# Kernel optimization log

Hardware: AMD Instinct MI355X
Metric: run time of the kernel (lower is better)

The kernel has to match this reference:

```python
import jax, jax.numpy as jnp
import numpy as np

B, L, N = 8, 5, 4096
RADIUS, K = 0.7, 32
SPATIAL_STRIDE = 16
TK, TSTRIDE = 3, 2  # temporal kernel / stride; temporal_padding=[1,1] replicate
DIM, DEPTH, HEADS, DIM_HEAD, MLP_DIM, OUT_DIM = 512, 5, 8, 64, 1024, 1088
INNER = HEADS * DIM_HEAD
N_ANCH = 64
NTOT = N + N_ANCH
M = NTOT // SPATIAL_STRIDE  # spatial anchors per output frame


def setup_inputs() -> dict:
    key = jax.random.key(0)
    ks = list(jax.random.split(key, 16))
    s = 0.02
    p = {}
    p["points"] = jax.random.uniform(ks[0], (B, L, N, 3), jnp.float32, -1.0, 1.0)
    p["conv_d_w"] = jax.random.normal(ks[1], (DIM, 4), jnp.float32) * s
    p["conv_f_w"] = jax.random.normal(ks[2], (DIM, 3), jnp.float32) * s
    p["pos_w"] = jax.random.normal(ks[3], (DIM, 4), jnp.float32) * s
    p["pos_b"] = jnp.zeros((DIM,), jnp.float32)
    p["ln1_g"] = jnp.ones((DEPTH, DIM)); p["ln1_b"] = jnp.zeros((DEPTH, DIM))
    p["qkv_w"] = jax.random.normal(ks[4], (DEPTH, DIM, 3 * INNER), jnp.float32) * s
    p["attn_out_w"] = jax.random.normal(ks[5], (DEPTH, INNER, DIM), jnp.float32) * s
    p["attn_out_b"] = jnp.zeros((DEPTH, DIM))
    p["ln2_g"] = jnp.ones((DEPTH, DIM)); p["ln2_b"] = jnp.zeros((DEPTH, DIM))
    p["ff1_w"] = jax.random.normal(ks[6], (DEPTH, DIM, MLP_DIM), jnp.float32) * s
    p["ff1_b"] = jnp.zeros((DEPTH, MLP_DIM))
    p["ff2_w"] = jax.random.normal(ks[7], (DEPTH, MLP_DIM, DIM), jnp.float32) * s
    p["ff2_b"] = jnp.zeros((DEPTH, DIM))
    p["head_ln_g"] = jnp.ones((DIM,)); p["head_ln_b"] = jnp.zeros((DIM,))
    p["head1_w"] = jax.random.normal(ks[8], (DIM, MLP_DIM), jnp.float32) * s
    p["head1_b"] = jnp.zeros((MLP_DIM,))
    p["head2_w"] = jax.random.normal(ks[9], (MLP_DIM, OUT_DIM), jnp.float32) * s
    p["head2_b"] = jnp.zeros((OUT_DIM,))
    return p


def _layer_norm(x, g, b, eps=1e-5):
    mu = jnp.mean(x, -1, keepdims=True)
    var = jnp.mean((x - mu) ** 2, -1, keepdims=True)
    return (x - mu) * jax.lax.rsqrt(var + eps) * g + b


def _anchor_grid():
    lin = jnp.linspace(-1.5, 1.5, 4)
    gx, gy, gz = jnp.meshgrid(lin, lin, lin, indexing="ij")
    return jnp.stack([gx.ravel(), gy.ravel(), gz.ravel()], -1)  # (64,3)


def _fps(pts, m):
    # furthest point sampling, pts (N,3) -> (m,) int32, first pick is index 0 (pointnet2 semantics)
    def step(carry, _):
        dist, last = carry
        d = jnp.sum((pts - pts[last]) ** 2, -1)
        dist = jnp.minimum(dist, d)
        return (dist, jnp.argmax(dist).astype(jnp.int32)), last
    init = (jnp.full((pts.shape[0],), 1e10, pts.dtype), jnp.int32(0))
    _, idx = jax.lax.scan(step, init, None, length=m)
    return idx


def _ball_query(anchors, pts, radius, k):
    # first k point indices within radius of each anchor; pad with first hit (0 if none)
    d2 = jnp.sum((anchors[:, None, :] - pts[None, :, :]) ** 2, -1)  # (M,N)
    n = pts.shape[0]
    cand = jnp.where(d2 < radius * radius, jnp.arange(n, dtype=jnp.int32), n)
    neg_topk, _ = jax.lax.top_k(-cand, k)  # k smallest indices, ascending
    idx = -neg_topk
    first = idx[:, :1]
    idx = jnp.where(idx == n, first, idx)
    return jnp.where(idx == n, 0, idx)


def _forward(points, conv_d_w, conv_f_w, pos_w, pos_b, ln1_g, ln1_b, qkv_w,
             attn_out_w, attn_out_b, ln2_g, ln2_b, ff1_w, ff1_b, ff2_w, ff2_b,
             head_ln_g, head_ln_b, head1_w, head1_b, head2_w, head2_b):
    anch = _anchor_grid()  # (64,3)
    pts = jnp.concatenate(
        [points[..., :3], jnp.broadcast_to(anch, (B, L, N_ANCH, 3))], axis=2)  # (B,L,NTOT,3)
    # replicate temporal padding [1,1]
    frames = jnp.concatenate([pts[:, :1], pts, pts[:, -1:]], axis=1)  # (B,L+2,NTOT,3)

    trad = (TK - 1) // 2
    nT = L + 2
    gather = jax.vmap(lambda p, i: p[i])
    out_xyz, out_feat = [], []
    for t in range(trad, nT - trad, TSTRIDE):
        f_t = frames[:, t]                                   # (B,NTOT,3)
        a_idx = jax.vmap(lambda p: _fps(p, M))(f_t)          # (B,M)
        a_xyz = gather(f_t, a_idx)                           # (B,M,3)
        feats_w = []
        for i in range(t - trad, t + trad + 1):
            nb = frames[:, i]                                # (B,NTOT,3)
            idx = jax.vmap(lambda a, p: _ball_query(a, p, RADIUS, K))(a_xyz, nb)  # (B,M,K)
            grouped = gather(nb, idx)                        # (B,M,K,3)
            disp = grouped - a_xyz[:, :, None, :]
            tdisp = jnp.full((B, M, K, 1), float(i - t), disp.dtype)
            disp4 = jnp.concatenate([disp, tdisp], -1)       # (B,M,K,4)
            # conv_f(features) + conv_d(displacement); features fed in are the xyz themselves
            feat = (jnp.einsum("bmkc,dc->bmkd", grouped, conv_f_w)
                    + jnp.einsum("bmkc,dc->bmkd", disp4, conv_d_w))
            feats_w.append(jnp.max(feat, axis=2))            # spatial max -> (B,M,DIM)
        out_feat.append(jnp.max(jnp.stack(feats_w, 0), axis=0))  # temporal max
        out_xyz.append(a_xyz)

    nF = len(out_xyz)
    xyzs = jnp.stack(out_xyz, 1)                             # (B,nF,M,3)
    feats = jnp.stack(out_feat, 1).reshape(B, nF * M, DIM)
    tcol = jnp.broadcast_to(
        jnp.arange(1, nF + 1, dtype=xyzs.dtype)[None, :, None, None], (B, nF, M, 1))
    xyzts = jnp.concatenate([xyzs, tcol], -1).reshape(B, nF * M, 4)
    x = jnp.einsum("bnc,dc->bnd", xyzts, pos_w) + pos_b + feats  # (B,T,DIM); emb_relu=False

    scale = DIM_HEAD ** -0.5
    for l in range(DEPTH):
        xn = _layer_norm(x, ln1_g[l], ln1_b[l])
        q, k, v = jnp.split(xn @ qkv_w[l], 3, axis=-1)
        rs = lambda a: a.reshape(B, -1, HEADS, DIM_HEAD)
        q, k, v = rs(q), rs(k), rs(v)
        att = jax.nn.softmax(jnp.einsum("bqhd,bkhd->bhqk", q, k) * scale, axis=-1)
        o = jnp.einsum("bhqk,bkhd->bqhd", att, v).reshape(B, -1, INNER)
        x = x + o @ attn_out_w[l] + attn_out_b[l]
        xn = _layer_norm(x, ln2_g[l], ln2_b[l])
        x = x + jax.nn.gelu(xn @ ff1_w[l] + ff1_b[l], approximate=False) @ ff2_w[l] + ff2_b[l]

    x = jnp.max(x, axis=1)                                   # (B,DIM)
    x = _layer_norm(x, head_ln_g, head_ln_b)
    x = jax.nn.gelu(x @ head1_w + head1_b, approximate=False) @ head2_w + head2_b
    x = x.reshape(B, 1, OUT_DIM // 64, 64)
    x = jax.nn.softmax(x, axis=-1)
    return x @ anch                                          # (B,1,J,3)


def reference(points, conv_d_w, conv_f_w, pos_w, pos_b, ln1_g, ln1_b, qkv_w,
              attn_out_w, attn_out_b, ln2_g, ln2_b, ff1_w, ff1_b, ff2_w, ff2_b,
              head_ln_g, head_ln_b, head1_w, head1_b, head2_w, head2_b):
    return _forward(points, conv_d_w, conv_f_w, pos_w, pos_b, ln1_g, ln1_b, qkv_w,
                    attn_out_w, attn_out_b, ln2_g, ln2_b, ff1_w, ff1_b, ff2_w, ff2_b,
                    head_ln_g, head_ln_b, head1_w, head1_b, head2_w, head2_b)
```

## Files before the change

### kernel.cpp

```cpp
#include <hip/hip_runtime.h>
#include <hip/hip_bf16.h>
#include <cstddef>

#define BB 8
#define LL 5
#define NN 4096
#define NANCH 64
#define NPTS 4160
#define MM 260
#define NFRAME 3
#define SSEQ 780
#define DIMC 512
#define NHEAD 8
#define DHEAD 64
#define MLPD 1024
#define OUTD 1088
#define NROWS 6240
#define VPITCH 784
#define WBUFSZ 2097152

typedef __attribute__((ext_vector_type(8))) short s16x8;
typedef __attribute__((ext_vector_type(4))) float fx4;
typedef unsigned short ushort_t;
typedef unsigned int uint_t;

__device__ __forceinline__ float sqdist_rn(float x1, float y1, float z1,
                                           float x2, float y2, float z2) {
    float dx = __fsub_rn(x1, x2);
    float dy = __fsub_rn(y1, y2);
    float dz = __fsub_rn(z1, z2);
    return __fadd_rn(__fadd_rn(__fmul_rn(dx, dx), __fmul_rn(dy, dy)), __fmul_rn(dz, dz));
}

__device__ __forceinline__ float gelu_exact(float v) {
    return 0.5f * v * (1.0f + erff(v * 0.70710678118654752440f));
}

__device__ __forceinline__ uint_t bf16rn(float f) {
    uint_t u = __float_as_uint(f);
    return (u + 0x7FFFu + ((u >> 16) & 1u)) >> 16;
}
__device__ __forceinline__ void split2(float f, ushort_t& h, ushort_t& l) {
    uint_t hb = bf16rn(f);
    h = (ushort_t)hb;
    float fh = __uint_as_float(hb << 16);
    l = (ushort_t)bf16rn(f - fh);
}

typedef __attribute__((address_space(3))) unsigned int as3u;
typedef const __attribute__((address_space(1))) unsigned int as1u;
__device__ __forceinline__ void gload16(const ushort_t* g, ushort_t* l) {
    __builtin_amdgcn_global_load_lds((as1u*)g, (as3u*)l, 16, 0, 0);
}

template <int CTRL>
__device__ __forceinline__ int dpp_mov(int v) {
    return __builtin_amdgcn_update_dpp(0, v, CTRL, 0xF, 0xF, true);
}
#define DPP_STEP_F(op, v, ctrl) v = op(v, __int_as_float(dpp_mov<ctrl>(__float_as_int(v))))
__device__ __forceinline__ float wave_max_bcast(float v) {
    DPP_STEP_F(fmaxf, v, 0x111); DPP_STEP_F(fmaxf, v, 0x112);
    DPP_STEP_F(fmaxf, v, 0x114); DPP_STEP_F(fmaxf, v, 0x118);
    DPP_STEP_F(fmaxf, v, 0x142); DPP_STEP_F(fmaxf, v, 0x143);
    return __int_as_float(__builtin_amdgcn_readlane(__float_as_int(v), 63));
}
__device__ __forceinline__ float faddf(float a, float b) { return a + b; }
__device__ __forceinline__ float wave_sum_bcast(float v) {
    DPP_STEP_F(faddf, v, 0x111); DPP_STEP_F(faddf, v, 0x112);
    DPP_STEP_F(faddf, v, 0x114); DPP_STEP_F(faddf, v, 0x118);
    DPP_STEP_F(faddf, v, 0x142); DPP_STEP_F(faddf, v, 0x143);
    return __int_as_float(__builtin_amdgcn_readlane(__float_as_int(v), 63));
}
__device__ __forceinline__ float row16_maxf(float v) {
    DPP_STEP_F(fmaxf, v, 0x111); DPP_STEP_F(fmaxf, v, 0x112);
    DPP_STEP_F(fmaxf, v, 0x114); DPP_STEP_F(fmaxf, v, 0x118);
    return __int_as_float(__builtin_amdgcn_readlane(__float_as_int(v), 15));
}

__device__ __forceinline__ void wsplit_tile(
    int bid, int tid, int nthr,
    const float* __restrict__ qkvw, const float* __restrict__ projw,
    const float* __restrict__ ff1w, const float* __restrict__ ff2w,
    ushort_t* __restrict__ th, ushort_t* __restrict__ tl,
    float (*T)[33]) {
    const float* src; int K, N; size_t dst;
    if (bid < 768)       { src = qkvw;  K = 512;  N = 1536; dst = 0;       }
    else if (bid < 1024) { src = projw; K = 512;  N = 512;  dst = 786432;  bid -= 768;  }
    else if (bid < 1536) { src = ff1w;  K = 512;  N = 1024; dst = 1048576; bid -= 1024; }
    else                 { src = ff2w;  K = 1024; N = 512;  dst = 1572864; bid -= 1536; }
    int ntn = N >> 5;
    int tn = bid % ntn, tk = bid / ntn;
    int n0 = tn * 32, k0 = tk * 32;
    for (int e = tid; e < 1024; e += nthr) {
        int r = e >> 5, c = e & 31;
        T[r][c] = src[(size_t)(k0 + r) * N + n0 + c];
    }
    __syncthreads();
    for (int e = tid; e < 1024; e += nthr) {
        int r = e >> 5, c = e & 31;
        ushort_t h, l;
        split2(T[c][r], h, l);
        th[dst + (size_t)(n0 + r) * K + k0 + c] = h;
        tl[dst + (size_t)(n0 + r) * K + k0 + c] = l;
    }
}

__global__ __launch_bounds__(256) void build_pts_kernel(const float* __restrict__ points,
                                                        float* __restrict__ pts) {
    int i = blockIdx.x * 256 + threadIdx.x;
    if (i >= BB * LL * NPTS) return;
    int n = i % NPTS;
    int bl = i / NPTS;
    if (n < NN) {
        const float* src = points + ((size_t)bl * NN + n) * 3;
        pts[(size_t)i * 3 + 0] = src[0];
        pts[(size_t)i * 3 + 1] = src[1];
        pts[(size_t)i * 3 + 2] = src[2];
    } else {
        int j = n - NN;
        int ix = j >> 4, iy = (j >> 2) & 3, iz = j & 3;
        pts[(size_t)i * 3 + 0] = -1.5f + (float)ix;
        pts[(size_t)i * 3 + 1] = -1.5f + (float)iy;
        pts[(size_t)i * 3 + 2] = -1.5f + (float)iz;
    }
}

__global__ __launch_bounds__(256) void fps_ws_kernel(
    const float* __restrict__ pts, float* __restrict__ axyz,
    const float* __restrict__ qkvw, const float* __restrict__ projw,
    const float* __restrict__ ff1w, const float* __restrict__ ff2w,
    ushort_t* __restrict__ th, ushort_t* __restrict__ tl) {
    __shared__ __align__(16) char smem[50048];
    int bid = blockIdx.x;
    int tid = threadIdx.x;
    if (bid >= 24) {
        wsplit_tile(bid - 24, tid, 256, qkvw, projw, ff1w, ff2w, th, tl,
                    (float(*)[33])smem);
        return;
    }
    float* sx = (float*)smem;
    float* sy = sx + NPTS;
    float* sz = sy + NPTS;
    float* redv = sz + NPTS;
    int* redi = (int*)(redv + 8);

    int b = bid / 3, f = bid % 3;
    const float* P = pts + (size_t)(b * LL + 2 * f) * NPTS * 3;
    int lane = tid & 63, wid = tid >> 6;
    int start = tid < 64 ? 17 * tid : 1088 + 16 * (tid - 64);
    float px[17], py[17], pz[17], dist[17];
#pragma unroll
    for (int j = 0; j < 16; j++) {
        int n = start + j;
        float gx = P[(size_t)n * 3 + 0];
        float gy = P[(size_t)n * 3 + 1];
        float gz = P[(size_t)n * 3 + 2];
        px[j] = gx; py[j] = gy; pz[j] = gz;
        sx[n] = gx; sy[n] = gy; sz[n] = gz;
        dist[j] = 1e10f;
    }
    if (tid < 64) {
        int n = start + 16;
        float gx = P[(size_t)n * 3 + 0];
        float gy = P[(size_t)n * 3 + 1];
        float gz = P[(size_t)n * 3 + 2];
        px[16] = gx; py[16] = gy; pz[16] = gz;
        sx[n] = gx; sy[n] = gy; sz[n] = gz;
        dist[16] = 1e10f;
    } else {
        px[16] = 0.f; py[16] = 0.f; pz[16] = 0.f;
        dist[16] = -1.0f;
    }
    __syncthreads();
    float ax = sx[0], ay = sy[0], az = sz[0];
    float* out = axyz + (size_t)bid * MM * 3;
    for (int m = 0; m < MM; m++) {
        if (tid == 0) { out[m * 3 + 0] = ax; out[m * 3 + 1] = ay; out[m * 3 + 2] = az; }
        float bv = -1.0f;
        int bjn = start;
#pragma unroll
        for (int j = 0; j < 16; j++) {
            float d = sqdist_rn(px[j], py[j], pz[j], ax, ay, az);
            float dj = fminf(dist[j], d);
            dist[j] = dj;
            if (dj > bv) { bv = dj; bjn = start + j; }
        }
        if (tid < 64) {
            float d = sqdist_rn(px[16], py[16], pz[16], ax, ay, az);
            float dj = fminf(dist[16], d);
            dist[16] = dj;
            if (dj > bv) { bv = dj; bjn = start + 16; }
        }
        float wmv = wave_max_bcast(bv);
        unsigned long long mk = __ballot(bv == wmv);
        int srcl = __ffsll(mk) - 1;
        int wn = __builtin_amdgcn_readlane(bjn, srcl);
        int par = (m & 1) * 4;
        if (lane == 0) { redv[par + wid] = wmv; redi[par + wid] = wn; }
        __syncthreads();
        float b0 = redv[par + 0], b1 = redv[par + 1];
        float b2 = redv[par + 2], b3 = redv[par + 3];
        int i0 = redi[par + 0], i1 = redi[par + 1];
        int i2 = redi[par + 2], i3 = redi[par + 3];
        float bb = b0; int bn = i0;
        if (b1 > bb) { bb = b1; bn = i1; }
        if (b2 > bb) { bb = b2; bn = i2; }
        if (b3 > bb) { bb = b3; bn = i3; }
        ax = sx[bn]; ay = sy[bn]; az = sz[bn];
    }
}

__global__ __launch_bounds__(64) void group_conv_kernel(
    const float* __restrict__ pts, const float* __restrict__ axyz,
    const float* __restrict__ conv_d_w, const float* __restrict__ conv_f_w,
    const float* __restrict__ pos_w, const float* __restrict__ pos_b,
    float* __restrict__ x) {
    int gid = blockIdx.x;
    int b = gid / SSEQ;
    int rem = gid % SSEQ;
    int f = rem / MM;
    int lane = threadIdx.x;
    const float* A = axyz + (size_t)gid * 3;
    float ax = A[0], ay = A[1], az = A[2];

    float cf0[8], cf1[8], cf2[8], cd0[8], cd1[8], cd2[8], cd3[8], fmx[8];
#pragma unroll
    for (int c = 0; c < 8; c++) {
        int d = lane + 64 * c;
        cf0[c] = conv_f_w[d * 3 + 0];
        cf1[c] = conv_f_w[d * 3 + 1];
        cf2[c] = conv_f_w[d * 3 + 2];
        cd0[c] = conv_d_w[d * 4 + 0];
        cd1[c] = conv_d_w[d * 4 + 1];
        cd2[c] = conv_d_w[d * 4 + 2];
        cd3[c] = conv_d_w[d * 4 + 3];
        fmx[c] = -INFINITY;
    }
    __shared__ int nbr[32];
    __shared__ float gxs[32], gys[32], gzs[32];
    const float R2 = 0.49000000953674316f;

    for (int wi = 0; wi < 3; wi++) {
        int l = 2 * f + wi - 1;
        l = l < 0 ? 0 : (l > 4 ? 4 : l);
        const float* P = pts + (size_t)(b * LL + l) * NPTS * 3;
        int cnt = 0;
        for (int base = 0; base < NPTS && cnt < 32; base += 64) {
            int n = base + lane;
            float d2 = sqdist_rn(P[(size_t)n * 3], P[(size_t)n * 3 + 1], P[(size_t)n * 3 + 2],
                                 ax, ay, az);
            bool hit = d2 < R2;
            unsigned long long mk = __ballot(hit);
            int rank = (int)__popcll(mk & (((unsigned long long)1 << lane) - 1ull));
            if (hit && (cnt + rank) < 32) nbr[cnt + rank] = n;
            cnt += (int)__popcll(mk);
        }
        __syncthreads();
        int eff = cnt < 32 ? cnt : 32;
        if (lane < 32) {
            int idx = (eff == 0) ? 0 : (lane < eff ? nbr[lane] : nbr[0]);
            gxs[lane] = P[(size_t)idx * 3 + 0];
            gys[lane] = P[(size_t)idx * 3 + 1];
            gzs[lane] = P[(size_t)idx * 3 + 2];
        }
        __syncthreads();
        float tf = (float)(wi - 1);
        for (int k = 0; k < 32; k++) {
            float gx = gxs[k], gy = gys[k], gz = gzs[k];
            float dx = gx - ax, dy = gy - ay, dz = gz - az;
#pragma unroll
            for (int c = 0; c < 8; c++) {
                float v = gx * cf0[c] + gy * cf1[c] + gz * cf2[c] +
                          dx * cd0[c] + dy * cd1[c] + dz * cd2[c] + tf * cd3[c];
                fmx[c] = fmaxf(fmx[c], v);
            }
        }
        __syncthreads();
    }
    float tcol = (float)(f + 1);
#pragma unroll
    for (int c = 0; c < 8; c++) {
        int d = lane + 64 * c;
        float pos = ax * pos_w[d * 4 + 0] + ay * pos_w[d * 4 + 1] +
                    az * pos_w[d * 4 + 2] + tcol * pos_w[d * 4 + 3] + pos_b[d];
        x[(size_t)gid * DIMC + d] = fmx[c] + pos;
    }
}

__global__ __launch_bounds__(64) void ln_kernel(const float* __restrict__ x,
                                                const float* __restrict__ g,
                                                const float* __restrict__ b,
                                                ushort_t* __restrict__ yh,
                                                ushort_t* __restrict__ yl) {
    int r = blockIdx.x;
    int lane = threadIdx.x;
    const float* xr = x + (size_t)r * DIMC;
    float4 v0 = *(const float4*)(xr + lane * 8);
    float4 v1 = *(const float4*)(xr + lane * 8 + 4);
    float s = v0.x + v0.y + v0.z + v0.w + v1.x + v1.y + v1.z + v1.w;
    s = wave_sum_bcast(s);
    float mean = s * (1.0f / 512.0f);
    float dv[8];
    dv[0] = v0.x - mean; dv[1] = v0.y - mean; dv[2] = v0.z - mean; dv[3] = v0.w - mean;
    dv[4] = v1.x - mean; dv[5] = v1.y - mean; dv[6] = v1.z - mean; dv[7] = v1.w - mean;
    float sq = 0.f;
#pragma unroll
    for (int c = 0; c < 8; c++) sq += dv[c] * dv[c];
    sq = wave_sum_bcast(sq);
    float var = sq * (1.0f / 512.0f);
    float inv = 1.0f / sqrtf(var + 1e-5f);
    int d = lane * 8;
    ushort_t hs[8], ls[8];
#pragma unroll
    for (int c = 0; c < 8; c++) {
        float v = dv[c] * inv * g[d + c] + b[d + c];
        split2(v, hs[c], ls[c]);
    }
    uint4 hv, lv;
    hv.x = hs[0] | ((uint_t)hs[1] << 16); hv.y = hs[2] | ((uint_t)hs[3] << 16);
    hv.z = hs[4] | ((uint_t)hs[5] << 16); hv.w = hs[6] | ((uint_t)hs[7] << 16);
    lv.x = ls[0] | ((uint_t)ls[1] << 16); lv.y = ls[2] | ((uint_t)ls[3] << 16);
    lv.z = ls[4] | ((uint_t)ls[5] << 16); lv.w = ls[6] | ((uint_t)ls[7] << 16);
    *(uint4*)(yh + (size_t)r * DIMC + d) = hv;
    *(uint4*)(yl + (size_t)r * DIMC + d) = lv;
}

#define BK 32

template <int BN, int EPI>
__global__ __launch_bounds__(256) void gemm_mfma(
    const ushort_t* __restrict__ Ahg, const ushort_t* __restrict__ Alg,
    const ushort_t* __restrict__ Bhg, const ushort_t* __restrict__ Blg,
    const float* __restrict__ bias, const float* __restrict__ R,
    float* __restrict__ C, ushort_t* __restrict__ Ch, ushort_t* __restrict__ Cl,
    ushort_t* __restrict__ Vh, ushort_t* __restrict__ Vl,
    int M, int N, int K) {
    const int WN = BN / 2, NT = WN / 16;
    __shared__ __align__(16) ushort_t Ah[128 * BK];
    __shared__ __align__(16) ushort_t Al[128 * BK];
    __shared__ __align__(16) ushort_t Bh[BN * BK];
    __shared__ __align__(16) ushort_t Bl[BN * BK];
    int tid = threadIdx.x;
    int lane = tid & 63, w = tid >> 6;
    int wm = w & 1, wn = w >> 1;
    int quad = lane >> 4, l15 = lane & 15;

    int nx = gridDim.x;
    int nwg = nx * gridDim.y;
    int lid = blockIdx.x + nx * blockIdx.y;
    int q = nwg >> 3, r = nwg & 7;
    int xcd = lid & 7, off = lid >> 3;
    int nid = (xcd < r ? xcd * (q + 1) : r * (q + 1) + (xcd - r) * q) + off;
    int m0 = (nid / nx) * 128, n0 = (nid % nx) * BN;

    int sr = lane >> 2;
    int sc = lane & 3;
    int kq = ((sc ^ ((sr >> 1) & 3)) << 3);

    int aoff[2];
#pragma unroll
    for (int i = 0; i < 2; i++) {
        int g = w + 4 * i;
        int row = m0 + g * 16 + sr; if (row >= M) row = M - 1;
        aoff[i] = row * K + kq;
    }
    int boff[BN == 128 ? 2 : 1];
    if (BN == 128) {
#pragma unroll
        for (int i = 0; i < 2; i++) {
            int g = w + 4 * i;
            boff[i] = (n0 + g * 16 + sr) * K + kq;
        }
    } else {
        boff[0] = (n0 + w * 16 + sr) * K + kq;
    }

    fx4 acc[4][NT];
#pragma unroll
    for (int mi = 0; mi < 4; mi++)
#pragma unroll
        for (int nj = 0; nj < NT; nj++) acc[mi][nj] = (fx4){0.f, 0.f, 0.f, 0.f};

    int rsw = (l15 >> 1) & 3;
    int aro = (64 * wm + l15) * BK + ((quad ^ rsw) << 3);
    int bro = (WN * wn + l15) * BK + ((quad ^ rsw) << 3);

    for (int k0 = 0; k0 < K; k0 += BK) {
#pragma unroll
        for (int i = 0; i < 2; i++) {
            int g = w + 4 * i;
            gload16(Ahg + aoff[i] + k0, &Ah[g * 16 * BK]);
            gload16(Alg + aoff[i] + k0, &Al[g * 16 * BK]);
        }
        if (BN == 128) {
#pragma unroll
            for (int i = 0; i < 2; i++) {
                int g = w + 4 * i;
                gload16(Bhg + boff[i] + k0, &Bh[g * 16 * BK]);
                gload16(Blg + boff[i] + k0, &Bl[g * 16 * BK]);
            }
        } else {
            gload16(Bhg + boff[0] + k0, &Bh[w * 16 * BK]);
            gload16(Blg + boff[0] + k0, &Bl[w * 16 * BK]);
        }
        __syncthreads();

        s16x8 bf[NT][2];
#pragma unroll
        for (int nj = 0; nj < NT; nj++) {
            bf[nj][0] = *(const s16x8*)&Bh[bro + 16 * nj * BK];
            bf[nj][1] = *(const s16x8*)&Bl[bro + 16 * nj * BK];
        }
#pragma unroll
        for (int mi = 0; mi < 4; mi++) {
            s16x8 aH = *(const s16x8*)&Ah[aro + 16 * mi * BK];
            s16x8 aL = *(const s16x8*)&Al[aro + 16 * mi * BK];
#pragma unroll
            for (int nj = 0; nj < NT; nj++) {
                acc[mi][nj] = __builtin_amdgcn_mfma_f32_16x16x32_bf16(aH, bf[nj][0], acc[mi][nj], 0, 0, 0);
                acc[mi][nj] = __builtin_amdgcn_mfma_f32_16x16x32_bf16(aH, bf[nj][1], acc[mi][nj], 0, 0, 0);
                acc[mi][nj] = __builtin_amdgcn_mfma_f32_16x16x32_bf16(aL, bf[nj][0], acc[mi][nj], 0, 0, 0);
            }
        }
        __syncthreads();
    }
#pragma unroll
    for (int mi = 0; mi < 4; mi++) {
#pragma unroll
        for (int r2 = 0; r2 < 4; r2++) {
            int row = m0 + 64 * wm + 16 * mi + quad * 4 + r2;
            if (row < M) {
#pragma unroll
                for (int nj = 0; nj < NT; nj++) {
                    int col = n0 + WN * wn + 16 * nj + l15;
                    float v = acc[mi][nj][r2];
                    if (EPI == 0) {
                        C[(size_t)row * N + col] = v;
                    } else if (EPI == 3) {
                        C[(size_t)row * N + col] = v + bias[col] + R[(size_t)row * N + col];
                    } else if (EPI == 2) {
                        float gv = gelu_exact(v + bias[col]);
                        ushort_t h, l;
                        split2(gv, h, l);
                        Ch[(size_t)row * N + col] = h;
                        Cl[(size_t)row * N + col] = l;
                    } else if (EPI == 5) {
                        ushort_t h, l;
                        split2(v, h, l);
                        if (col < 1024) {
                            Ch[(size_t)row * 1024 + col] = h;
                            Cl[(size_t)row * 1024 + col] = l;
                        } else {
                            int bb = row / SSEQ, key = row % SSEQ;
                            int hh = (col - 1024) >> 6, dd = (col - 1024) & 63;
                            size_t vo = ((size_t)((bb * 8 + hh) * 64 + dd)) * VPITCH + key;
                            Vh[vo] = h;
                            Vl[vo] = l;
                        }
                    }
                }
            }
        }
    }
}

#define KP2 64
#define PP 72
#define NATTN 832

__global__ __launch_bounds__(256, 2) void attn_mfma_kernel(
    const ushort_t* __restrict__ qkh, const ushort_t* __restrict__ qkl,
    const ushort_t* __restrict__ vth, const ushort_t* __restrict__ vtl,
    ushort_t* __restrict__ oh, ushort_t* __restrict__ ol,
    const float* __restrict__ nqkvw, const float* __restrict__ nprojw,
    const float* __restrict__ nff1w, const float* __restrict__ nff2w,
    ushort_t* __restrict__ nth, ushort_t* __restrict__ ntl) {
    __shared__ __align__(16) char smem[67584];
    int lid = blockIdx.x;
    if (lid >= NATTN) {
        wsplit_tile(lid - NATTN, threadIdx.x, 256, nqkvw, nprojw, nff1w, nff2w,
                    nth, ntl, (float(*)[33])smem);
        return;
    }
    int xcd = lid & 7, idx = lid >> 3;
    int qt = idx % 13;
    int bh = xcd * 8 + idx / 13;
    int b = bh >> 3, h = bh & 7;

    ushort_t* Qh  = (ushort_t*)smem;
    ushort_t* Ql  = Qh + 64 * KP2;
    ushort_t* Kh  = Ql + 64 * KP2;
    ushort_t* Kl  = Kh + 64 * KP2;
    ushort_t* Vth = Kl + 64 * KP2;
    ushort_t* Vtl = Vth + 64 * KP2;
    ushort_t* Ph  = Vtl + 64 * KP2;
    ushort_t* Pl  = Ph + 64 * PP;

    int tid = threadIdx.x;
    int lane = tid & 63, w = tid >> 6;
    int quad = lane >> 4, l15 = lane & 15;

    int q0 = qt * 64;
    int nq = SSEQ - q0; if (nq > 64) nq = 64;

    int sr8 = lane >> 3;
    int csw = (lane & 7) ^ sr8;

#pragma unroll
    for (int i = 0; i < 2; i++) {
        int grp = i * 4 + w;
        int row = grp * 8 + sr8;
        int gq = q0 + (row < nq ? row : nq - 1);
        size_t go = (size_t)(b * SSEQ + gq) * 1024 + h * 64 + csw * 8;
        gload16(qkh + go, Qh + grp * 512);
        gload16(qkl + go, Ql + grp * 512);
    }

    fx4 accO[4];
#pragma unroll
    for (int dj = 0; dj < 4; dj++) accO[dj] = (fx4){0.f, 0.f, 0.f, 0.f};
    fx4 accL = (fx4){0.f, 0.f, 0.f, 0.f};

    s16x8 ones;
#pragma unroll
    for (int j = 0; j < 8; j++) ones[j] = (short)16256;

    int r7 = l15 & 7;
    int c0 = (quad ^ r7) * 8;
    int c1 = ((quad ^ r7) ^ 4) * 8;

    for (int kt = 0; kt < 13; kt++) {
        int k0 = kt * 64;
        int nk = SSEQ - k0; if (nk > 64) nk = 64;
        __syncthreads();
#pragma unroll
        for (int i = 0; i < 2; i++) {
            int grp = i * 4 + w;
            int row = grp * 8 + sr8;
            int gk = k0 + (row < nk ? row : nk - 1);
            size_t go = (size_t)(b * SSEQ + gk) * 1024 + h * 64 + 512 + csw * 8;
            gload16(qkh + go, Kh + grp * 512);
            gload16(qkl + go, Kl + grp * 512);
            size_t vo = ((size_t)(bh * 64 + row)) * VPITCH + k0 + csw * 8;
            gload16(vth + vo, Vth + grp * 512);
            gload16(vtl + vo, Vtl + grp * 512);
        }
        __syncthreads();

        fx4 accS[4];
#pragma unroll
        for (int nj = 0; nj < 4; nj++) accS[nj] = (fx4){0.f, 0.f, 0.f, 0.f};
#pragma unroll
        for (int ks = 0; ks < 2; ks++) {
            int ca = ks ? c1 : c0;
            s16x8 aH = *(const s16x8*)&Qh[(16 * w + l15) * KP2 + ca];
            s16x8 aL = *(const s16x8*)&Ql[(16 * w + l15) * KP2 + ca];
#pragma unroll
            for (int nj = 0; nj < 4; nj++) {
                s16x8 bH = *(const s16x8*)&Kh[(16 * nj + l15) * KP2 + ca];
                s16x8 bL = *(const s16x8*)&Kl[(16 * nj + l15) * KP2 + ca];
                accS[nj] = __builtin_amdgcn_mfma_f32_16x16x32_bf16(aH, bH, accS[nj], 0, 0, 0);
                accS[nj] = __builtin_amdgcn_mfma_f32_16x16x32_bf16(aH, bL, accS[nj], 0, 0, 0);
                accS[nj] = __builtin_amdgcn_mfma_f32_16x16x32_bf16(aL, bH, accS[nj], 0, 0, 0);
            }
        }
#pragma unroll
        for (int nj = 0; nj < 4; nj++) {
            int key = 16 * nj + l15;
            bool valid = key < nk;
#pragma unroll
            for (int r = 0; r < 4; r++) {
                float s = accS[nj][r] * 0.125f;
                float p = valid ? __expf(s) : 0.f;
                ushort_t hh, ll;
                split2(p, hh, ll);
                int qrow = 16 * w + quad * 4 + r;
                Ph[qrow * PP + key] = hh;
                Pl[qrow * PP + key] = ll;
            }
        }
#pragma unroll
        for (int ks = 0; ks < 2; ks++) {
            int ca = ks ? c1 : c0;
            s16x8 aPh = *(const s16x8*)&Ph[(16 * w + l15) * PP + 32 * ks + quad * 8];
            s16x8 aPl = *(const s16x8*)&Pl[(16 * w + l15) * PP + 32 * ks + quad * 8];
            accL = __builtin_amdgcn_mfma_f32_16x16x32_bf16(aPh, ones, accL, 0, 0, 0);
            accL = __builtin_amdgcn_mfma_f32_16x16x32_bf16(aPl, ones, accL, 0, 0, 0);
#pragma unroll
            for (int dj = 0; dj < 4; dj++) {
                s16x8 bVh = *(const s16x8*)&Vth[(16 * dj + l15) * KP2 + ca];
                s16x8 bVl = *(const s16x8*)&Vtl[(16 * dj + l15) * KP2 + ca];
                accO[dj] = __builtin_amdgcn_mfma_f32_16x16x32_bf16(aPh, bVh, accO[dj], 0, 0, 0);
                accO[dj] = __builtin_amdgcn_mfma_f32_16x16x32_bf16(aPh, bVl, accO[dj], 0, 0, 0);
                accO[dj] = __builtin_amdgcn_mfma_f32_16x16x32_bf16(aPl, bVh, accO[dj], 0, 0, 0);
            }
        }
    }
#pragma unroll
    for (int r = 0; r < 4; r++) {
        int lq = 16 * w + quad * 4 + r;
        if (lq < nq) {
            float inv = 1.0f / accL[r];
            size_t base = (size_t)(b * SSEQ + q0 + lq) * DIMC + h * 64 + l15;
#pragma unroll
            for (int dj = 0; dj < 4; dj++) {
                ushort_t hh, ll;
                split2(accO[dj][r] * inv, hh, ll);
                oh[base + 16 * dj] = hh;
                ol[base + 16 * dj] = ll;
            }
        }
    }
}

__global__ __launch_bounds__(512) void pool_max_kernel(const float* __restrict__ x,
                                                       float* __restrict__ partial) {
    int c = blockIdx.x;
    int bb = blockIdx.y;
    int d = threadIdx.x;
    const float* xb = x + ((size_t)(bb * SSEQ + c * 60)) * DIMC + d;
    float m = -INFINITY;
#pragma unroll 4
    for (int s = 0; s < 60; s++) m = fmaxf(m, xb[(size_t)s * DIMC]);
    partial[((size_t)bb * 13 + c) * DIMC + d] = m;
}

__global__ __launch_bounds__(512) void pool_ln_kernel(const float* __restrict__ partial,
                                                      const float* __restrict__ g,
                                                      const float* __restrict__ b,
                                                      float* __restrict__ out) {
    int bb = blockIdx.x;
    int d = threadIdx.x;
    const float* pb = partial + (size_t)bb * 13 * DIMC + d;
    float m = -INFINITY;
#pragma unroll
    for (int c = 0; c < 13; c++) m = fmaxf(m, pb[(size_t)c * DIMC]);
    __shared__ float col[512];
    __shared__ float red[512];
    col[d] = m;
    red[d] = m;
    __syncthreads();
    for (int s = 256; s > 0; s >>= 1) {
        if (d < s) red[d] += red[d + s];
        __syncthreads();
    }
    float mean = red[0] * (1.0f / 512.0f);
    __syncthreads();
    float dv = col[d] - mean;
    red[d] = dv * dv;
    __syncthreads();
    for (int s = 256; s > 0; s >>= 1) {
        if (d < s) red[d] += red[d + s];
        __syncthreads();
    }
    float var = red[0] * (1.0f / 512.0f);
    float inv = 1.0f / sqrtf(var + 1e-5f);
    out[(size_t)bb * DIMC + d] = dv * inv * g[d] + b[d];
}

__global__ __launch_bounds__(256) void head1_kernel(const float* __restrict__ in,
                                                    const float* __restrict__ W,
                                                    const float* __restrict__ bias,
                                                    float* __restrict__ out) {
    int g = blockIdx.x, bb = blockIdx.y;
    int tid = threadIdx.x;
    int c = tid & 63, ks = tid >> 6;
    int col = g * 64 + c;
    __shared__ float xr[512];
    xr[tid] = in[(size_t)bb * 512 + tid];
    xr[tid + 256] = in[(size_t)bb * 512 + tid + 256];
    __syncthreads();
    float acc = 0.f;
    const float* Wc = W + col;
    for (int k = ks * 128; k < ks * 128 + 128; k++)
        acc += xr[k] * Wc[(size_t)k * MLPD];
    __shared__ float red[256];
    red[tid] = acc;
    __syncthreads();
    if (ks == 0) {
        float v = red[c] + red[c + 64] + red[c + 128] + red[c + 192] + bias[col];
        out[(size_t)bb * MLPD + col] = gelu_exact(v);
    }
}

__global__ __launch_bounds__(256) void head2_kernel(const float* __restrict__ in,
                                                    const float* __restrict__ W,
                                                    const float* __restrict__ bias,
                                                    float* __restrict__ out) {
    int g = blockIdx.x, bb = blockIdx.y;
    int tid = threadIdx.x;
    int c = tid & 63, ks = tid >> 6;
    int col = g * 64 + c;
    __shared__ float xr[1024];
    xr[tid] = in[(size_t)bb * 1024 + tid];
    xr[tid + 256] = in[(size_t)bb * 1024 + tid + 256];
    xr[tid + 512] = in[(size_t)bb * 1024 + tid + 512];
    xr[tid + 768] = in[(size_t)bb * 1024 + tid + 768];
    __syncthreads();
    float acc = 0.f;
    const float* Wc = W + col;
    for (int k = ks * 256; k < ks * 256 + 256; k++)
        acc += xr[k] * Wc[(size_t)k * OUTD];
    __shared__ float red[256];
    red[tid] = acc;
    __syncthreads();
    if (ks == 0) {
        out[(size_t)bb * OUTD + col] = red[c] + red[c + 64] + red[c + 128] + red[c + 192] + bias[col];
    }
}

__global__ __launch_bounds__(64) void smax_anchor_kernel(const float* __restrict__ h2,
                                                         float* __restrict__ out) {
    int bb = blockIdx.x / 17;
    int gcol = blockIdx.x % 17;
    int j = threadIdx.x;
    float v = h2[(size_t)bb * OUTD + gcol * 64 + j];
    float mx = wave_max_bcast(v);
    float p = expf(v - mx);
    float sum = wave_sum_bcast(p);
    int ix = j >> 4, iy = (j >> 2) & 3, iz = j & 3;
    float sx = wave_sum_bcast(p * (-1.5f + (float)ix));
    float sy = wave_sum_bcast(p * (-1.5f + (float)iy));
    float sz = wave_sum_bcast(p * (-1.5f + (float)iz));
    if (j == 0) {
        float* o = out + ((size_t)bb * 17 + gcol) * 3;
        o[0] = sx / sum;
        o[1] = sy / sum;
        o[2] = sz / sum;
    }
}

extern "C" void kernel_launch(void* const* d_in, const int* in_sizes, int n_in,
                              void* d_out, int out_size, void* d_ws, size_t ws_size,
                              hipStream_t stream) {
    const float* points     = (const float*)d_in[0];
    const float* conv_d_w   = (const float*)d_in[1];
    const float* conv_f_w   = (const float*)d_in[2];
    const float* pos_w      = (const float*)d_in[3];
    const float* pos_b      = (const float*)d_in[4];
    const float* ln1_g      = (const float*)d_in[5];
    const float* ln1_b      = (const float*)d_in[6];
    const float* qkv_w      = (const float*)d_in[7];
    const float* attn_out_w = (const float*)d_in[8];
    const float* attn_out_b = (const float*)d_in[9];
    const float* ln2_g      = (const float*)d_in[10];
    const float* ln2_b      = (const float*)d_in[11];
    const float* ff1_w      = (const float*)d_in[12];
    const float* ff1_b      = (const float*)d_in[13];
    const float* ff2_w      = (const float*)d_in[14];
    const float* ff2_b      = (const float*)d_in[15];
    const float* head_ln_g  = (const float*)d_in[16];
    const float* head_ln_b  = (const float*)d_in[17];
    const float* head1_w    = (const float*)d_in[18];
    const float* head1_b    = (const float*)d_in[19];
    const float* head2_w    = (const float*)d_in[20];
    const float* head2_b    = (const float*)d_in[21];

    float* ws = (float*)d_ws;
    float* pts    = ws;
    float* axyz   = pts + 499200;
    float* xbuf   = axyz + 18720;
    float* qkvreg = xbuf + 3194880;
    float* pooled = qkvreg + 9601024;
    float* h1     = pooled + 4096;
    float* h2     = h1 + 8192;
    float* fend   = h2 + 8704;
    ushort_t* qkh = (ushort_t*)qkvreg;
    ushort_t* qkl = qkh + 6389760;
    ushort_t* vth = qkl + 6389760;
    ushort_t* vtl = vth + 3211264;
    ushort_t* us   = (ushort_t*)fend;
    ushort_t* xnh  = us;
    ushort_t* xnl  = xnh + 3194880;
    ushort_t* atth = xnl + 3194880;
    ushort_t* attl = atth + 3194880;
    ushort_t* ffhh = attl + 3194880;
    ushort_t* ffhl = ffhh + 6389760;
    ushort_t* wbh  = ffhl + 6389760;
    ushort_t* wbl  = wbh + 2 * WBUFSZ;
    float* ppart = qkvreg;

    build_pts_kernel<<<650, 256, 0, stream>>>(points, pts);
    fps_ws_kernel<<<24 + 2048, 256, 0, stream>>>(
        pts, axyz, qkv_w, attn_out_w, ff1_w, ff2_w, wbh, wbl);
    group_conv_kernel<<<NROWS, 64, 0, stream>>>(pts, axyz, conv_d_w, conv_f_w,
                                                pos_w, pos_b, xbuf);
    const int MB = (NROWS + 127) / 128;
    for (int l = 0; l < 5; l++) {
        ushort_t* wth = wbh + (size_t)(l & 1) * WBUFSZ;
        ushort_t* wtl = wbl + (size_t)(l & 1) * WBUFSZ;
        ushort_t* nth = wbh + (size_t)((l + 1) & 1) * WBUFSZ;
        ushort_t* ntl = wbl + (size_t)((l + 1) & 1) * WBUFSZ;
        int ln2off = l * 512;
        ln_kernel<<<NROWS, 64, 0, stream>>>(xbuf, ln1_g + ln2off, ln1_b + ln2off, xnh, xnl);
        gemm_mfma<128, 5><<<dim3(1536 / 128, MB), 256, 0, stream>>>(
            xnh, xnl, wth, wtl, nullptr, nullptr, nullptr, qkh, qkl, vth, vtl,
            NROWS, 1536, 512);
        int lnx = l + 1;
        attn_mfma_kernel<<<dim3(l < 4 ? NATTN + 2048 : NATTN), 256, 0, stream>>>(
            qkh, qkl, vth, vtl, atth, attl,
            l < 4 ? qkv_w + (size_t)lnx * 512 * 1536 : nullptr,
            l < 4 ? attn_out_w + (size_t)lnx * 512 * 512 : nullptr,
            l < 4 ? ff1_w + (size_t)lnx * 512 * 1024 : nullptr,
            l < 4 ? ff2_w + (size_t)lnx * 1024 * 512 : nullptr,
            nth, ntl);
        gemm_mfma<64, 3><<<dim3(512 / 64, MB), 256, 0, stream>>>(
            atth, attl, wth + 786432, wtl + 786432, attn_out_b + ln2off, xbuf,
            xbuf, nullptr, nullptr, nullptr, nullptr, NROWS, 512, 512);
        ln_kernel<<<NROWS, 64, 0, stream>>>(xbuf, ln2_g + ln2off, ln2_b + ln2off, xnh, xnl);
        gemm_mfma<128, 2><<<dim3(1024 / 128, MB), 256, 0, stream>>>(
            xnh, xnl, wth + 1048576, wtl + 1048576, ff1_b + l * 1024, nullptr,
            nullptr, ffhh, ffhl, nullptr, nullptr, NROWS, 1024, 512);
        gemm_mfma<64, 3><<<dim3(512 / 64, MB), 256, 0, stream>>>(
            ffhh, ffhl, wth + 1572864, wtl + 1572864, ff2_b + ln2off, xbuf,
            xbuf, nullptr, nullptr, nullptr, nullptr, NROWS, 512, 1024);
    }
    pool_max_kernel<<<dim3(13, BB), 512, 0, stream>>>(xbuf, ppart);
    pool_ln_kernel<<<BB, 512, 0, stream>>>(ppart, head_ln_g, head_ln_b, pooled);
    head1_kernel<<<dim3(16, BB), 256, 0, stream>>>(pooled, head1_w, head1_b, h1);
    head2_kernel<<<dim3(17, BB), 256, 0, stream>>>(h1, head2_w, head2_b, h2);
    smax_anchor_kernel<<<BB * 17, 64, 0, stream>>>(h2, (float*)d_out);
}
```

Baseline: 1.821 ms.

## Enlarge attention query tile to 128 rows with 8 waves and register-held Q

The attention kernel now uses 512-thread blocks, with each block covering 128 query rows instead of 64. The grid therefore shrinks from 832 to 448 attention blocks. Q fragments are loaded straight into registers rather than staged in shared memory. Each K/V tile is now reused by twice as many queries, so K/V global traffic drops, but fewer blocks run and register and LDS pressure per block goes up. The fused weight-split tiles also run with 512 threads.

```diff
diff --git a/kernel.cpp b/kernel.cpp
--- a/kernel.cpp
+++ b/kernel.cpp
@@ -70,11 +70,6 @@
     DPP_STEP_F(faddf, v, 0x114); DPP_STEP_F(faddf, v, 0x118);
     DPP_STEP_F(faddf, v, 0x142); DPP_STEP_F(faddf, v, 0x143);
     return __int_as_float(__builtin_amdgcn_readlane(__float_as_int(v), 63));
-}
-__device__ __forceinline__ float row16_maxf(float v) {
-    DPP_STEP_F(fmaxf, v, 0x111); DPP_STEP_F(fmaxf, v, 0x112);
-    DPP_STEP_F(fmaxf, v, 0x114); DPP_STEP_F(fmaxf, v, 0x118);
-    return __int_as_float(__builtin_amdgcn_readlane(__float_as_int(v), 15));
 }
 
 __device__ __forceinline__ void wsplit_tile(
@@ -466,64 +461,64 @@
 
 #define KP2 64
 #define PP 72
-#define NATTN 832
-
-__global__ __launch_bounds__(256, 2) void attn_mfma_kernel(
+#define NATTN 448
+
+__global__ __launch_bounds__(512, 4) void attn_mfma_kernel(
     const ushort_t* __restrict__ qkh, const ushort_t* __restrict__ qkl,
     const ushort_t* __restrict__ vth, const ushort_t* __restrict__ vtl,
     ushort_t* __restrict__ oh, ushort_t* __restrict__ ol,
     const float* __restrict__ nqkvw, const float* __restrict__ nprojw,
     const float* __restrict__ nff1w, const float* __restrict__ nff2w,
     ushort_t* __restrict__ nth, ushort_t* __restrict__ ntl) {
-    __shared__ __align__(16) char smem[67584];
+    __shared__ __align__(16) char smem[69632];
     int lid = blockIdx.x;
     if (lid >= NATTN) {
-        wsplit_tile(lid - NATTN, threadIdx.x, 256, nqkvw, nprojw, nff1w, nff2w,
+        wsplit_tile(lid - NATTN, threadIdx.x, 512, nqkvw, nprojw, nff1w, nff2w,
                     nth, ntl, (float(*)[33])smem);
         return;
     }
     int xcd = lid & 7, idx = lid >> 3;
-    int qt = idx % 13;
-    int bh = xcd * 8 + idx / 13;
+    int qt = idx % 7;
+    int bh = xcd * 8 + idx / 7;
     int b = bh >> 3, h = bh & 7;
 
-    ushort_t* Qh  = (ushort_t*)smem;
-    ushort_t* Ql  = Qh + 64 * KP2;
-    ushort_t* Kh  = Ql + 64 * KP2;
+    ushort_t* Kh  = (ushort_t*)smem;
     ushort_t* Kl  = Kh + 64 * KP2;
     ushort_t* Vth = Kl + 64 * KP2;
     ushort_t* Vtl = Vth + 64 * KP2;
     ushort_t* Ph  = Vtl + 64 * KP2;
-    ushort_t* Pl  = Ph + 64 * PP;
+    ushort_t* Pl  = Ph + 128 * PP;
 
     int tid = threadIdx.x;
     int lane = tid & 63, w = tid >> 6;
     int quad = lane >> 4, l15 = lane & 15;
 
-    int q0 = qt * 64;
-    int nq = SSEQ - q0; if (nq > 64) nq = 64;
+    int q0 = qt * 128;
+    int nq = SSEQ - q0; if (nq > 128) nq = 128;
+
+    s16x8 qfh[2], qfl[2];
+    {
+        int row = 16 * w + l15;
+        int gq = q0 + (row < nq ? row : nq - 1);
+        size_t go = (size_t)(b * SSEQ + gq) * 1024 + h * 64;
+#pragma unroll
+        for (int ks = 0; ks < 2; ks++) {
+            qfh[ks] = *(const s16x8*)(qkh + go + 32 * ks + quad * 8);
+            qfl[ks] = *(const s16x8*)(qkl + go + 32 * ks + quad * 8);
+        }
+    }
+
+    fx4 accO[4];
+#pragma unroll
+    for (int dj = 0; dj < 4; dj++) accO[dj] = (fx4){0.f, 0.f, 0.f, 0.f};
+    fx4 accL = (fx4){0.f, 0.f, 0.f, 0.f};
+
+    s16x8 ones;
+#pragma unroll
+    for (int j = 0; j < 8; j++) ones[j] = (short)16256;
 
     int sr8 = lane >> 3;
     int csw = (lane & 7) ^ sr8;
-
-#pragma unroll
-    for (int i = 0; i < 2; i++) {
-        int grp = i * 4 + w;
-        int row = grp * 8 + sr8;
-        int gq = q0 + (row < nq ? row : nq - 1);
-        size_t go = (size_t)(b * SSEQ + gq) * 1024 + h * 64 + csw * 8;
-        gload16(qkh + go, Qh + grp * 512);
-        gload16(qkl + go, Ql + grp * 512);
-    }
-
-    fx4 accO[4];
-#pragma unroll
-    for (int dj = 0; dj < 4; dj++) accO[dj] = (fx4){0.f, 0.f, 0.f, 0.f};
-    fx4 accL = (fx4){0.f, 0.f, 0.f, 0.f};
-
-    s16x8 ones;
-#pragma unroll
-    for (int j = 0; j < 8; j++) ones[j] = (short)16256;
 
     int r7 = l15 & 7;
     int c0 = (quad ^ r7) * 8;
@@ -533,17 +528,15 @@
         int k0 = kt * 64;
         int nk = SSEQ - k0; if (nk > 64) nk = 64;
         __syncthreads();
-#pragma unroll
-        for (int i = 0; i < 2; i++) {
-            int grp = i * 4 + w;
-            int row = grp * 8 + sr8;
+        {
+            int row = w * 8 + sr8;
             int gk = k0 + (row < nk ? row : nk - 1);
             size_t go = (size_t)(b * SSEQ + gk) * 1024 + h * 64 + 512 + csw * 8;
-            gload16(qkh + go, Kh + grp * 512);
-            gload16(qkl + go, Kl + grp * 512);
+            gload16(qkh + go, Kh + w * 512);
+            gload16(qkl + go, Kl + w * 512);
             size_t vo = ((size_t)(bh * 64 + row)) * VPITCH + k0 + csw * 8;
-            gload16(vth + vo, Vth + grp * 512);
-            gload16(vtl + vo, Vtl + grp * 512);
+            gload16(vth + vo, Vth + w * 512);
+            gload16(vtl + vo, Vtl + w * 512);
         }
         __syncthreads();
 
@@ -553,8 +546,8 @@
 #pragma unroll
         for (int ks = 0; ks < 2; ks++) {
             int ca = ks ? c1 : c0;
-            s16x8 aH = *(const s16x8*)&Qh[(16 * w + l15) * KP2 + ca];
-            s16x8 aL = *(const s16x8*)&Ql[(16 * w + l15) * KP2 + ca];
+            s16x8 aH = qfh[ks];
+            s16x8 aL = qfl[ks];
 #pragma unroll
             for (int nj = 0; nj < 4; nj++) {
                 s16x8 bH = *(const s16x8*)&Kh[(16 * nj + l15) * KP2 + ca];
@@ -797,7 +790,7 @@
             xnh, xnl, wth, wtl, nullptr, nullptr, nullptr, qkh, qkl, vth, vtl,
             NROWS, 1536, 512);
         int lnx = l + 1;
-        attn_mfma_kernel<<<dim3(l < 4 ? NATTN + 2048 : NATTN), 256, 0, stream>>>(
+        attn_mfma_kernel<<<dim3(l < 4 ? NATTN + 2048 : NATTN), 512, 0, stream>>>(
             qkh, qkl, vth, vtl, atth, attl,
             l < 4 ? qkv_w + (size_t)lnx * 512 * 1536 : nullptr,
             l < 4 ? attn_out_w + (size_t)lnx * 512 * 512 : nullptr,
```

Result: faster. 1.757 ms (-3.5%).
